# Performance work log

Hardware: AMD Instinct MI355X
Metric: run time of the kernel (lower is better)

The kernel has to match this reference:

```python
import jax, jax.numpy as jnp
import numpy as np

B = 65536          # batch
C = 16             # num_concepts
D = 64             # dim_per_concept
G = 32             # g_dim

def setup_inputs() -> dict:
    key = jax.random.key(0)
    ks = jax.random.split(key, 6)
    x  = jax.random.normal(ks[0], (B, C, D), dtype=jnp.float32)
    # DAG adjacency (zeros in torch init; use small random values for a nontrivial baseline)
    A  = 0.1 * jax.random.normal(ks[1], (C, C), dtype=jnp.float32)
    # Stacked per-concept 2-layer MLP weights (nets_z), torch Linear convention: W @ x + b
    W1 = jax.random.normal(ks[2], (C, G, D), dtype=jnp.float32) / np.sqrt(D)
    b1 = jax.random.normal(ks[3], (C, G), dtype=jnp.float32) * 0.01
    W2 = jax.random.normal(ks[4], (C, D, G), dtype=jnp.float32) / np.sqrt(G)
    b2 = jax.random.normal(ks[5], (C, D), dtype=jnp.float32) * 0.01
    return {"x": x, "A": A, "W1": W1, "b1": b1, "W2": W2, "b2": b2}

def reference(x, A, W1, b1, W2, b2):
    # mask: m[b,i,d] = sum_j A[j,i] * x[b,j,d]   (A.t() @ x)
    m = jnp.einsum('ji,bjd->bid', A, x)
    # g_z: per-concept Linear(D->G) -> ELU -> Linear(G->D), batched over concepts
    h = jax.nn.elu(jnp.einsum('cgd,bcd->bcg', W1, m) + b1[None, :, :])
    out = jnp.einsum('cdg,bcg->bcd', W2, h) + b2[None, :, :]
    return out  # [B, C, D]
```

## Files before the change

### kernel.cpp

```cpp
#include <hip/hip_runtime.h>
#include <hip/hip_fp16.h>

#define BATCH   65536
#define NC      16
#define DDIM    64
#define GDIM    32
#define TILE    64

extern "C" __global__ void __launch_bounds__(1024, 4)
causal_dag_kernel(const float* __restrict__ x, const float* __restrict__ A,
                  const float* __restrict__ W1, const float* __restrict__ b1,
                  const float* __restrict__ W2, const float* __restrict__ b2,
                  float* __restrict__ out)
{
    __shared__ __align__(16) unsigned char smem_raw[65536];
    __half* xs  = (__half*)smem_raw;
    float*  osf = (float*)smem_raw;

    const int t    = threadIdx.x;
    const int b0   = blockIdx.x * TILE;
    const int w    = __builtin_amdgcn_readfirstlane(t >> 6);
    const int lane = t & 63;
    const int sw   = lane & 7;

    const float* W1c = W1 + w * (GDIM * DDIM);
    const float* W2c = W2 + w * (DDIM * GDIM);
    const float* b1c = b1 + w * GDIM;
    const float* b2c = b2 + w * DDIM;

    float hacc[GDIM];
#pragma unroll
    for (int g = 0; g < GDIM; ++g) hacc[g] = b1c[g];

    for (int jh = 0; jh < 2; ++jh) {
#pragma unroll
        for (int p = 0; p < 8; ++p) {
            int f4 = p * 1024 + t;
            int bb = f4 >> 7;
            int r  = f4 & 127;
            int jp = r >> 4;
            int d4 = r & 15;
            const float4 v = *(const float4*)(
                x + ((size_t)(b0 + bb) * (NC * DDIM) + (jh * 8 + jp) * DDIM + d4 * 4));
            union { __half2 h2[2]; uint2 u; } pk;
            pk.h2[0] = __floats2half2_rn(v.x, v.y);
            pk.h2[1] = __floats2half2_rn(v.z, v.w);
            int dst = bb * 512 + jp * 64 + (((d4 >> 1) ^ (bb & 7)) << 3) + ((d4 & 1) << 2);
            *(uint2*)(xs + dst) = pk.u;
        }
        __syncthreads();

        float a[8];
#pragma unroll
        for (int jp = 0; jp < 8; ++jp) a[jp] = A[(jh * 8 + jp) * NC + w];

        const __half* xb = xs + lane * 512;
#pragma unroll
        for (int dq = 0; dq < 8; ++dq) {
            float mc[8];
#pragma unroll
            for (int k = 0; k < 8; ++k) mc[k] = 0.f;
#pragma unroll
            for (int jp = 0; jp < 8; ++jp) {
                uint4 q = *(const uint4*)(xb + jp * 64 + ((dq ^ sw) << 3));
                float2 f0 = __half22float2(*(__half2*)&q.x);
                float2 f1 = __half22float2(*(__half2*)&q.y);
                float2 f2 = __half22float2(*(__half2*)&q.z);
                float2 f3 = __half22float2(*(__half2*)&q.w);
                mc[0] = fmaf(a[jp], f0.x, mc[0]);
                mc[1] = fmaf(a[jp], f0.y, mc[1]);
                mc[2] = fmaf(a[jp], f1.x, mc[2]);
                mc[3] = fmaf(a[jp], f1.y, mc[3]);
                mc[4] = fmaf(a[jp], f2.x, mc[4]);
                mc[5] = fmaf(a[jp], f2.y, mc[5]);
                mc[6] = fmaf(a[jp], f3.x, mc[6]);
                mc[7] = fmaf(a[jp], f3.y, mc[7]);
            }
            const int d0 = dq * 8;
#pragma unroll
            for (int g = 0; g < GDIM; ++g) {
                float acc = hacc[g];
                acc = fmaf(W1c[g * DDIM + d0 + 0], mc[0], acc);
                acc = fmaf(W1c[g * DDIM + d0 + 1], mc[1], acc);
                acc = fmaf(W1c[g * DDIM + d0 + 2], mc[2], acc);
                acc = fmaf(W1c[g * DDIM + d0 + 3], mc[3], acc);
                acc = fmaf(W1c[g * DDIM + d0 + 4], mc[4], acc);
                acc = fmaf(W1c[g * DDIM + d0 + 5], mc[5], acc);
                acc = fmaf(W1c[g * DDIM + d0 + 6], mc[6], acc);
                acc = fmaf(W1c[g * DDIM + d0 + 7], mc[7], acc);
                hacc[g] = acc;
            }
        }
        if (jh == 0) __syncthreads();
    }

#pragma unroll
    for (int g = 0; g < GDIM; ++g)
        hacc[g] = hacc[g] > 0.f ? hacc[g] : (__expf(hacc[g]) - 1.f);

    for (int r = 0; r < 4; ++r) {
        float och[16];
#pragma unroll
        for (int i = 0; i < 16; ++i) {
            const int d = r * 16 + i;
            float acc = b2c[d];
#pragma unroll
            for (int g = 0; g < GDIM; ++g)
                acc = fmaf(W2c[d * GDIM + g], hacc[g], acc);
            och[i] = acc;
        }
        __syncthreads();
#pragma unroll
        for (int s = 0; s < 4; ++s) {
            const int slot = ((w << 2) + s) ^ lane;
            *(float4*)(osf + lane * 256 + (slot << 2)) = *(const float4*)(och + s * 4);
        }
        __syncthreads();
#pragma unroll
        for (int k = 0; k < 4; ++k) {
            const int f   = k * 1024 + t;
            const int b   = f >> 6;
            const int rem = f & 63;
            const int c   = rem >> 2;
            const int s   = rem & 3;
            const float4 v = *(const float4*)(osf + b * 256 + ((rem ^ b) << 2));
            *(float4*)(out + (size_t)(b0 + b) * (NC * DDIM) + c * DDIM + r * 16 + s * 4) = v;
        }
    }
}

extern "C" void kernel_launch(void* const* d_in, const int* in_sizes, int n_in,
                              void* d_out, int out_size, void* d_ws, size_t ws_size,
                              hipStream_t stream) {
    const float* x  = (const float*)d_in[0];
    const float* A  = (const float*)d_in[1];
    const float* W1 = (const float*)d_in[2];
    const float* b1 = (const float*)d_in[3];
    const float* W2 = (const float*)d_in[4];
    const float* b2 = (const float*)d_in[5];
    float* out = (float*)d_out;

    causal_dag_kernel<<<BATCH / TILE, 1024, 0, stream>>>(x, A, W1, b1, W2, b2, out);
}
```

Before: 1.259 ms.

## Stage W1/W2 weights as fp16 in LDS and swizzle x tile concept index

Weights W1 and W2 are converted to half precision and staged in a second 64KB LDS region, so the inner loops read them with 128-bit LDS loads instead of scalar global/constant loads. The x tile layout adds an XOR swizzle on the concept index to reduce LDS bank conflicts. LDS use per block doubles to 128KB, limiting occupancy to one block per CU, and weight precision drops to fp16.

New measurement: 1.568 ms. +24.5%, slower.

```diff
diff --git a/kernel.cpp b/kernel.cpp
--- a/kernel.cpp
+++ b/kernel.cpp
@@ -7,14 +7,15 @@
 #define GDIM    32
 #define TILE    64
 
-extern "C" __global__ void __launch_bounds__(1024, 4)
+extern "C" __global__ void __launch_bounds__(1024)
 causal_dag_kernel(const float* __restrict__ x, const float* __restrict__ A,
                   const float* __restrict__ W1, const float* __restrict__ b1,
                   const float* __restrict__ W2, const float* __restrict__ b2,
                   float* __restrict__ out)
 {
-    __shared__ __align__(16) unsigned char smem_raw[65536];
+    __shared__ __align__(16) unsigned char smem_raw[131072];
     __half* xs  = (__half*)smem_raw;
+    __half* wsh = (__half*)(smem_raw + 65536);
     float*  osf = (float*)smem_raw;
 
     const int t    = threadIdx.x;
@@ -22,15 +23,16 @@
     const int w    = __builtin_amdgcn_readfirstlane(t >> 6);
     const int lane = t & 63;
     const int sw   = lane & 7;
+    const int lhi  = (lane >> 3) & 7;
 
-    const float* W1c = W1 + w * (GDIM * DDIM);
-    const float* W2c = W2 + w * (DDIM * GDIM);
     const float* b1c = b1 + w * GDIM;
     const float* b2c = b2 + w * DDIM;
 
     float hacc[GDIM];
 #pragma unroll
     for (int g = 0; g < GDIM; ++g) hacc[g] = b1c[g];
+
+    const __half* w1w = wsh + w * (GDIM * DDIM);
 
     for (int jh = 0; jh < 2; ++jh) {
 #pragma unroll
@@ -45,8 +47,20 @@
             union { __half2 h2[2]; uint2 u; } pk;
             pk.h2[0] = __floats2half2_rn(v.x, v.y);
             pk.h2[1] = __floats2half2_rn(v.z, v.w);
-            int dst = bb * 512 + jp * 64 + (((d4 >> 1) ^ (bb & 7)) << 3) + ((d4 & 1) << 2);
+            int dst = bb * 512 + (jp ^ (bb >> 3)) * 64
+                    + (((d4 >> 1) ^ (bb & 7)) << 3) + ((d4 & 1) << 2);
             *(uint2*)(xs + dst) = pk.u;
+        }
+        if (jh == 0) {
+#pragma unroll
+            for (int p = 0; p < 8; ++p) {
+                int f4 = p * 1024 + t;
+                const float4 v = *(const float4*)(W1 + (size_t)f4 * 4);
+                union { __half2 h2[2]; uint2 u; } pk;
+                pk.h2[0] = __floats2half2_rn(v.x, v.y);
+                pk.h2[1] = __floats2half2_rn(v.z, v.w);
+                *(uint2*)(wsh + f4 * 4) = pk.u;
+            }
         }
         __syncthreads();
 
@@ -62,7 +76,7 @@
             for (int k = 0; k < 8; ++k) mc[k] = 0.f;
 #pragma unroll
             for (int jp = 0; jp < 8; ++jp) {
-                uint4 q = *(const uint4*)(xb + jp * 64 + ((dq ^ sw) << 3));
+                uint4 q = *(const uint4*)(xb + (jp ^ lhi) * 64 + ((dq ^ sw) << 3));
                 float2 f0 = __half22float2(*(__half2*)&q.x);
                 float2 f1 = __half22float2(*(__half2*)&q.y);
                 float2 f2 = __half22float2(*(__half2*)&q.z);
@@ -79,15 +93,17 @@
             const int d0 = dq * 8;
 #pragma unroll
             for (int g = 0; g < GDIM; ++g) {
+                uint4 qw = *(const uint4*)(w1w + g * DDIM + d0);
+                const __half* hv = (const __half*)&qw;
                 float acc = hacc[g];
-                acc = fmaf(W1c[g * DDIM + d0 + 0], mc[0], acc);
-                acc = fmaf(W1c[g * DDIM + d0 + 1], mc[1], acc);
-                acc = fmaf(W1c[g * DDIM + d0 + 2], mc[2], acc);
-                acc = fmaf(W1c[g * DDIM + d0 + 3], mc[3], acc);
-                acc = fmaf(W1c[g * DDIM + d0 + 4], mc[4], acc);
-                acc = fmaf(W1c[g * DDIM + d0 + 5], mc[5], acc);
-                acc = fmaf(W1c[g * DDIM + d0 + 6], mc[6], acc);
-                acc = fmaf(W1c[g * DDIM + d0 + 7], mc[7], acc);
+                acc = fmaf(__half2float(hv[0]), mc[0], acc);
+                acc = fmaf(__half2float(hv[1]), mc[1], acc);
+                acc = fmaf(__half2float(hv[2]), mc[2], acc);
+                acc = fmaf(__half2float(hv[3]), mc[3], acc);
+                acc = fmaf(__half2float(hv[4]), mc[4], acc);
+                acc = fmaf(__half2float(hv[5]), mc[5], acc);
+                acc = fmaf(__half2float(hv[6]), mc[6], acc);
+                acc = fmaf(__half2float(hv[7]), mc[7], acc);
                 hacc[g] = acc;
             }
         }
@@ -98,15 +114,36 @@
     for (int g = 0; g < GDIM; ++g)
         hacc[g] = hacc[g] > 0.f ? hacc[g] : (__expf(hacc[g]) - 1.f);
 
+    __syncthreads();
+
+#pragma unroll
+    for (int p = 0; p < 8; ++p) {
+        int f4 = p * 1024 + t;
+        const float4 v = *(const float4*)(W2 + (size_t)f4 * 4);
+        union { __half2 h2[2]; uint2 u; } pk;
+        pk.h2[0] = __floats2half2_rn(v.x, v.y);
+        pk.h2[1] = __floats2half2_rn(v.z, v.w);
+        *(uint2*)(wsh + f4 * 4) = pk.u;
+    }
+    __syncthreads();
+
+    const __half* w2w = wsh + w * (DDIM * GDIM);
+
     for (int r = 0; r < 4; ++r) {
-        float och[16];
+        __align__(16) float och[16];
 #pragma unroll
         for (int i = 0; i < 16; ++i) {
             const int d = r * 16 + i;
             float acc = b2c[d];
 #pragma unroll
-            for (int g = 0; g < GDIM; ++g)
-                acc = fmaf(W2c[d * GDIM + g], hacc[g], acc);
+            for (int gq = 0; gq < 4; ++gq) {
+                uint4 qw = *(const uint4*)(w2w + d * GDIM + gq * 8);
+                const __half* hv = (const __half*)&qw;
+                const int g0 = gq * 8;
+#pragma unroll
+                for (int k = 0; k < 8; ++k)
+                    acc = fmaf(__half2float(hv[k]), hacc[g0 + k], acc);
+            }
             och[i] = acc;
         }
         __syncthreads();
```
